# Optimization experiments

Hardware: AMD Instinct MI355X
Metric: run time of the kernel (lower is better)

## Reference

```python
import jax, jax.numpy as jnp
import numpy as np

B, L, D = 4, 4096, 128
BLOCK, SPARSITY = 64, 0.9
NEG = -1e9


def _make_block_mask(key):
    nb = L // BLOCK
    bm = jax.random.uniform(key, (nb, nb)) > SPARSITY
    bm = bm | jnp.eye(nb, dtype=bool)  # keep diagonal blocks so no row is fully masked
    bm = jnp.tril(bm)
    return jnp.repeat(jnp.repeat(bm, BLOCK, axis=0), BLOCK, axis=1)  # [L, L]


def _xavier(key, shape):
    limit = float(np.sqrt(6.0 / (shape[0] + shape[1])))
    return jax.random.uniform(key, shape, jnp.float32, -limit, limit)


def setup_inputs() -> dict:
    key = jax.random.key(0)
    ks = jax.random.split(key, 10)
    t = lambda k: jax.random.normal(k, (B, L, D), jnp.float32)
    return {
        'q_real': t(ks[0]), 'q_imag': t(ks[1]),
        'k_real': t(ks[2]), 'k_imag': t(ks[3]),
        'v_real': t(ks[4]), 'v_imag': t(ks[5]),
        'W_qkv': _xavier(ks[6], (6 * D, 6 * D)),
        'b_qkv': jnp.zeros((6 * D,), jnp.float32),
        'W_out': _xavier(ks[7], (2 * D, 2 * D)),
        'b_out': jnp.zeros((2 * D,), jnp.float32),
        'block_mask': _make_block_mask(ks[8]),
    }


def reference(q_real, q_imag, k_real, k_imag, v_real, v_imag,
              W_qkv, b_qkv, W_out, b_out, block_mask):
    d = q_real.shape[-1]
    scale = d ** -0.5
    # fused qkv projection over the 6 concatenated channels
    x = jnp.concatenate([q_real, q_imag, k_real, k_imag, v_real, v_imag], axis=-1)  # [B,L,6D]
    qkv = (x @ W_qkv.T + b_qkv).reshape(x.shape[0], x.shape[1], 6, d)
    q_r, q_i, k_r, k_i, v_r, v_i = (qkv[:, :, j] for j in range(6))

    def attn(q, k, v):
        s = jnp.einsum('bqd,bkd->bqk', q, k) * scale          # [B,L,L]
        s = jnp.where(block_mask[None], s, NEG)               # block-sparse mask
        a = jax.nn.softmax(s, axis=-1)                        # dropout = identity (eval)
        return jnp.einsum('bqk,bkd->bqd', a, v)

    out = jnp.concatenate([attn(q_r, k_r, v_r), attn(q_i, k_i, v_i)], axis=-1)  # [B,L,2D]
    out = out @ W_out.T + b_out
    return out[..., :d], out[..., d:]
```

## Files before the change

### kernel.cpp

```cpp
#include <hip/hip_runtime.h>
#include <hip/hip_bf16.h>

typedef unsigned short u16;
typedef __attribute__((ext_vector_type(8))) short bf16x8;
typedef __attribute__((ext_vector_type(4))) float f32x4;

#define SEQ_L 4096
#define M_TOT 16384

__device__ __forceinline__ float bf2f(u16 x) {
    unsigned u = ((unsigned)x) << 16;
    return __builtin_bit_cast(float, u);
}
__device__ __forceinline__ u16 f2bf(float f) {
    unsigned u = __builtin_bit_cast(unsigned, f);
    u += 0x7FFFu + ((u >> 16) & 1u);
    return (u16)(u >> 16);
}
__device__ __forceinline__ void gload16(const u16* g, u16* l) {
    __builtin_amdgcn_global_load_lds(
        (const __attribute__((address_space(1))) unsigned int*)g,
        (__attribute__((address_space(3))) unsigned int*)l, 16, 0, 0);
}

__global__ __launch_bounds__(256) void pack_x(
    const float* __restrict__ in0, const float* __restrict__ in1, const float* __restrict__ in2,
    const float* __restrict__ in3, const float* __restrict__ in4, const float* __restrict__ in5,
    u16* __restrict__ x) {
    const float* ins[6] = {in0, in1, in2, in3, in4, in5};
    int which = blockIdx.y;
    const float* src = ins[which];
    int g = blockIdx.x * 256 + threadIdx.x;
    int m = g >> 4, c8 = g & 15;
    const float* sp = src + (size_t)m * 128 + c8 * 8;
    float4 a = *(const float4*)sp;
    float4 b = *(const float4*)(sp + 4);
    u16 t[8] = {f2bf(a.x), f2bf(a.y), f2bf(a.z), f2bf(a.w),
                f2bf(b.x), f2bf(b.y), f2bf(b.z), f2bf(b.w)};
    *(uint4*)(x + (size_t)m * 768 + which * 128 + c8 * 8) = *(uint4*)t;
}

__global__ __launch_bounds__(256) void prep(
    const float* __restrict__ Wqkv, const float* __restrict__ Wout, const void* __restrict__ mask,
    u16* __restrict__ Wqkv_bf, u16* __restrict__ Wout_bf, unsigned char* __restrict__ cmask) {
    int id = blockIdx.x * 256 + threadIdx.x;
    if (id < 73728 + 8192) {
        const float* src = (id < 73728) ? Wqkv : Wout;
        u16* dst = (id < 73728) ? Wqkv_bf : Wout_bf;
        int i = (id < 73728) ? id : (id - 73728);
        const float* sp = src + (size_t)i * 8;
        float4 a = *(const float4*)sp;
        float4 b = *(const float4*)(sp + 4);
        u16 t[8] = {f2bf(a.x), f2bf(a.y), f2bf(a.z), f2bf(a.w),
                    f2bf(b.x), f2bf(b.y), f2bf(b.z), f2bf(b.w)};
        *(uint4*)(dst + (size_t)i * 8) = *(uint4*)t;
    } else if (id < 73728 + 8192 + 4096) {
        int i = id - 73728 - 8192;
        int bi = i >> 6, bj = i & 63;
        size_t e = (size_t)(bi * 64) * SEQ_L + (size_t)bj * 64;
        const unsigned char* p8 = (const unsigned char*)mask;
        unsigned w0 = *(const unsigned*)mask;
        bool v;
        if (w0 == 0x01010101u || w0 == 0xFFFFFFFFu)      v = p8[e] != 0;
        else if (w0 == 0x3F803F80u || w0 == 0x3C003C00u) v = ((const u16*)mask)[e] != 0;
        else                                             v = ((const unsigned*)mask)[e] != 0;
        cmask[i] = v ? 1 : 0;
    }
}

__global__ __launch_bounds__(256) void qkv_gemm(
    const u16* __restrict__ X, const u16* __restrict__ W, const float* __restrict__ bias,
    u16* __restrict__ qk, u16* __restrict__ vt) {
    __shared__ __align__(16) u16 As[128 * 64];
    __shared__ __align__(16) u16 Bs[128 * 64];
    int m0 = blockIdx.x * 128, n0 = blockIdx.y * 128;
    int tid = threadIdx.x, lane = tid & 63, w = tid >> 6;
    int ln = lane & 15, quad = lane >> 4;
    int rw = (w >> 1) * 64, cw = (w & 1) * 64;
    int lr8 = lane >> 3, lc = lane & 7;
    int swz_st = lc ^ (lr8 & 7);
    f32x4 acc[4][4] = {};
    for (int kk = 0; kk < 768; kk += 64) {
        __syncthreads();
        #pragma unroll
        for (int j = 0; j < 4; j++) {
            int r0 = w * 32 + j * 8;
            int r = r0 + lr8;
            gload16(X + (size_t)(m0 + r) * 768 + kk + swz_st * 8, As + r0 * 64 + lane * 8);
            gload16(W + (size_t)(n0 + r) * 768 + kk + swz_st * 8, Bs + r0 * 64 + lane * 8);
        }
        __syncthreads();
        #pragma unroll
        for (int s = 0; s < 2; s++) {
            bf16x8 af[4], bfr[4];
            #pragma unroll
            for (int i = 0; i < 4; i++) {
                int R = rw + i * 16 + ln;
                af[i] = *(const bf16x8*)(As + R * 64 + ((4 * s + quad) ^ (ln & 7)) * 8);
            }
            #pragma unroll
            for (int t = 0; t < 4; t++) {
                int R = cw + t * 16 + ln;
                bfr[t] = *(const bf16x8*)(Bs + R * 64 + ((4 * s + quad) ^ (ln & 7)) * 8);
            }
            #pragma unroll
            for (int i = 0; i < 4; i++)
                #pragma unroll
                for (int t = 0; t < 4; t++)
                    acc[i][t] = __builtin_amdgcn_mfma_f32_16x16x32_bf16(af[i], bfr[t], acc[i][t], 0, 0, 0);
        }
    }
    #pragma unroll
    for (int i = 0; i < 4; i++) {
        int row0 = m0 + rw + i * 16 + 4 * quad;
        #pragma unroll
        for (int t = 0; t < 4; t++) {
            int col = n0 + cw + t * 16 + ln;
            float bv = bias[col];
            if (col < 512) {
                #pragma unroll
                for (int r = 0; r < 4; r++)
                    qk[(size_t)(row0 + r) * 512 + col] = f2bf(acc[i][t][r] + bv);
            } else {
                int d = col - 512;
                int b = row0 >> 12, seq = row0 & 4095;
                u16 pk[4] = {f2bf(acc[i][t][0] + bv), f2bf(acc[i][t][1] + bv),
                             f2bf(acc[i][t][2] + bv), f2bf(acc[i][t][3] + bv)};
                *(ushort4*)(vt + ((size_t)(b * 2 + (d >> 7)) * 128 + (d & 127)) * SEQ_L + seq)
                    = *(ushort4*)pk;
            }
        }
    }
}

__global__ __launch_bounds__(256) void attn_kernel(
    const u16* __restrict__ qk, const u16* __restrict__ vt,
    const unsigned char* __restrict__ cmask, u16* __restrict__ attn_out) {
    __shared__ __align__(16) u16 Ks[2][64 * 128];
    __shared__ __align__(16) u16 Vt[2][128 * 64];
    __shared__ __align__(16) u16 Ps[4][16 * 72];

    int idx = blockIdx.x;
    int qi = 63 - (idx >> 3);
    int sub = idx & 7, c = sub & 1, b = sub >> 1;
    int tid = threadIdx.x, lane = tid & 63, w = tid >> 6;
    int ln = lane & 15, quad = lane >> 4;
    const float scale = 0.08838834764831845f;

    const u16* kb_base = qk + (size_t)b * SEQ_L * 512 + 256 + c * 128;
    const u16* vt_base = vt + (size_t)(b * 2 + c) * 128 * SEQ_L;

    int k_lr = lane >> 4, k_lc = lane & 15;
    int v_lr = lane >> 3, v_lc = lane & 7;

    bf16x8 qf[4];
    {
        size_t grow = (size_t)(b * SEQ_L + qi * 64 + w * 16 + ln);
        const u16* qp = qk + grow * 512 + c * 128;
        #pragma unroll
        for (int s = 0; s < 4; s++) qf[s] = *(const bf16x8*)(qp + 32 * s + 8 * quad);
    }
    float m_st[4], l_st[4];
    #pragma unroll
    for (int r = 0; r < 4; r++) { m_st[r] = -1e30f; l_st[r] = 0.f; }
    f32x4 accO[8] = {};

    const unsigned char* mrow = cmask + qi * 64;
    unsigned long long bm = 0;
    for (int k = 0; k <= qi; k++) bm |= (unsigned long long)(mrow[k] != 0) << k;

    int cur = __ffsll(bm) - 1; bm &= bm - 1;
    int buf = 0;
    {
        const u16* kp = kb_base + (size_t)cur * 64 * 512;
        const u16* vp = vt_base + cur * 64;
        #pragma unroll
        for (int j = 0; j < 4; j++) {
            int kr0 = w * 16 + j * 4, kr = kr0 + k_lr;
            gload16(kp + (size_t)kr * 512 + (k_lc ^ (kr & 7)) * 8, Ks[0] + kr0 * 128 + lane * 8);
            int vr0 = w * 32 + j * 8, vr = vr0 + v_lr;
            gload16(vp + (size_t)vr * SEQ_L + (v_lc ^ (vr & 7)) * 8, Vt[0] + vr0 * 64 + lane * 8);
        }
    }
    while (cur >= 0) {
        int nxt = bm ? (__ffsll(bm) - 1) : -1;
        if (bm) bm &= bm - 1;
        __syncthreads();
        if (nxt >= 0) {
            const u16* kp = kb_base + (size_t)nxt * 64 * 512;
            const u16* vp = vt_base + nxt * 64;
            #pragma unroll
            for (int j = 0; j < 4; j++) {
                int kr0 = w * 16 + j * 4, kr = kr0 + k_lr;
                gload16(kp + (size_t)kr * 512 + (k_lc ^ (kr & 7)) * 8, Ks[buf ^ 1] + kr0 * 128 + lane * 8);
                int vr0 = w * 32 + j * 8, vr = vr0 + v_lr;
                gload16(vp + (size_t)vr * SEQ_L + (v_lc ^ (vr & 7)) * 8, Vt[buf ^ 1] + vr0 * 64 + lane * 8);
            }
        }

        f32x4 accS[4] = {};
        #pragma unroll
        for (int s = 0; s < 4; s++) {
            #pragma unroll
            for (int t = 0; t < 4; t++) {
                int R = t * 16 + ln;
                bf16x8 bfr = *(const bf16x8*)(Ks[buf] + R * 128 + ((4 * s + quad) ^ (ln & 7)) * 8);
                accS[t] = __builtin_amdgcn_mfma_f32_16x16x32_bf16(qf[s], bfr, accS[t], 0, 0, 0);
            }
        }

        float P[4][4];
        #pragma unroll
        for (int r = 0; r < 4; r++) {
            float sv[4];
            float mx = -1e30f;
            #pragma unroll
            for (int t = 0; t < 4; t++) { sv[t] = accS[t][r] * scale; mx = fmaxf(mx, sv[t]); }
            #pragma unroll
            for (int off = 1; off < 16; off <<= 1) mx = fmaxf(mx, __shfl_xor(mx, off, 64));
            float nm = fmaxf(m_st[r], mx);
            float alpha = __expf(m_st[r] - nm);
            m_st[r] = nm;
            float rs = 0.f;
            #pragma unroll
            for (int t = 0; t < 4; t++) { float p = __expf(sv[t] - nm); P[t][r] = p; rs += p; }
            #pragma unroll
            for (int off = 1; off < 16; off <<= 1) rs += __shfl_xor(rs, off, 64);
            l_st[r] = l_st[r] * alpha + rs;
            #pragma unroll
            for (int nt = 0; nt < 8; nt++) accO[nt][r] *= alpha;
        }
        #pragma unroll
        for (int t = 0; t < 4; t++)
            #pragma unroll
            for (int r = 0; r < 4; r++)
                Ps[w][(4 * quad + r) * 72 + ln + 16 * t] = f2bf(P[t][r]);

        #pragma unroll
        for (int s2 = 0; s2 < 2; s2++) {
            bf16x8 pf = *(const bf16x8*)(&Ps[w][ln * 72 + 32 * s2 + 8 * quad]);
            #pragma unroll
            for (int nt = 0; nt < 8; nt++) {
                int R = nt * 16 + ln;
                bf16x8 vf = *(const bf16x8*)(Vt[buf] + R * 64 + ((4 * s2 + quad) ^ (ln & 7)) * 8);
                accO[nt] = __builtin_amdgcn_mfma_f32_16x16x32_bf16(pf, vf, accO[nt], 0, 0, 0);
            }
        }
        cur = nxt; buf ^= 1;
    }

    #pragma unroll
    for (int nt = 0; nt < 8; nt++) {
        int col = c * 128 + nt * 16 + ln;
        #pragma unroll
        for (int r = 0; r < 4; r++) {
            int row = b * SEQ_L + qi * 64 + w * 16 + 4 * quad + r;
            float inv = 1.0f / fmaxf(l_st[r], 1e-20f);
            attn_out[(size_t)row * 256 + col] = f2bf(accO[nt][r] * inv);
        }
    }
}

__global__ __launch_bounds__(256) void out_gemm(
    const u16* __restrict__ A, const u16* __restrict__ W, const float* __restrict__ bias,
    float* __restrict__ out) {
    __shared__ __align__(16) u16 As[64 * 64];
    __shared__ __align__(16) u16 Bs[64 * 64];
    int m0 = blockIdx.x * 64, n0 = blockIdx.y * 64;
    int tid = threadIdx.x, lane = tid & 63, w = tid >> 6;
    int ln = lane & 15, quad = lane >> 4;
    int lr8 = lane >> 3, lc = lane & 7;
    int swz_st = lc ^ (lr8 & 7);
    f32x4 acc[4] = {};
    for (int kk = 0; kk < 256; kk += 64) {
        __syncthreads();
        #pragma unroll
        for (int j = 0; j < 2; j++) {
            int r0 = w * 16 + j * 8;
            int r = r0 + lr8;
            gload16(A + (size_t)(m0 + r) * 256 + kk + swz_st * 8, As + r0 * 64 + lane * 8);
            gload16(W + (size_t)(n0 + r) * 256 + kk + swz_st * 8, Bs + r0 * 64 + lane * 8);
        }
        __syncthreads();
        #pragma unroll
        for (int s = 0; s < 2; s++) {
            int R = w * 16 + ln;
            bf16x8 af = *(const bf16x8*)(As + R * 64 + ((4 * s + quad) ^ (ln & 7)) * 8);
            #pragma unroll
            for (int t = 0; t < 4; t++) {
                int Rb = t * 16 + ln;
                bf16x8 bfr = *(const bf16x8*)(Bs + Rb * 64 + ((4 * s + quad) ^ (ln & 7)) * 8);
                acc[t] = __builtin_amdgcn_mfma_f32_16x16x32_bf16(af, bfr, acc[t], 0, 0, 0);
            }
        }
    }
    const size_t half = (size_t)M_TOT * 128;
    #pragma unroll
    for (int t = 0; t < 4; t++) {
        int col = n0 + t * 16 + ln;
        float bv = bias[col];
        float* base = (col < 128) ? (out + col) : (out + half + (col - 128));
        #pragma unroll
        for (int r = 0; r < 4; r++) {
            int row = m0 + w * 16 + 4 * quad + r;
            base[(size_t)row * 128] = acc[t][r] + bv;
        }
    }
}

extern "C" void kernel_launch(void* const* d_in, const int* in_sizes, int n_in,
                              void* d_out, int out_size, void* d_ws, size_t ws_size,
                              hipStream_t stream) {
    char* ws = (char*)d_ws;
    u16* x_bf    = (u16*)ws;
    u16* qk_buf  = x_bf + (size_t)M_TOT * 768;
    u16* vt_buf  = qk_buf + (size_t)M_TOT * 512;
    u16* attn_bf = vt_buf + (size_t)1024 * SEQ_L;
    u16* Wqkv_bf = attn_bf + (size_t)M_TOT * 256;
    u16* Wout_bf = Wqkv_bf + 589824;
    unsigned char* cmask = (unsigned char*)(Wout_bf + 65536);

    hipLaunchKernelGGL(pack_x, dim3(1024, 6), dim3(256), 0, stream,
                       (const float*)d_in[0], (const float*)d_in[1], (const float*)d_in[2],
                       (const float*)d_in[3], (const float*)d_in[4], (const float*)d_in[5], x_bf);
    hipLaunchKernelGGL(prep, dim3(336), dim3(256), 0, stream,
                       (const float*)d_in[6], (const float*)d_in[8], d_in[10],
                       Wqkv_bf, Wout_bf, cmask);
    hipLaunchKernelGGL(qkv_gemm, dim3(128, 6), dim3(256), 0, stream,
                       x_bf, Wqkv_bf, (const float*)d_in[7], qk_buf, vt_buf);
    hipLaunchKernelGGL(attn_kernel, dim3(512), dim3(256), 0, stream,
                       qk_buf, vt_buf, cmask, attn_bf);
    hipLaunchKernelGGL(out_gemm, dim3(256, 4), dim3(256), 0, stream,
                       attn_bf, Wout_bf, (const float*)d_in[9], (float*)d_out);
}
```

Baseline: 224.0 us.

## Fuse output projection into attention kernel and merge prep kernels

The attention kernel now processes both real and imaginary channels per block, keeping the normalized output in shared memory, then performs the output projection with W_out directly and writes fp32 results. The separate out_gemm kernel and the bf16 attention intermediate buffer are removed, and pack_x and prep are combined into one launch. This saves a launch and an HBM round trip of the attention output. In exchange, the grid halves to 256 blocks with serialized per-channel work, and the larger shared memory footprint can lower occupancy, so load balance across CUs may get worse.

```diff
diff --git a/kernel.cpp b/kernel.cpp
--- a/kernel.cpp
+++ b/kernel.cpp
@@ -23,39 +23,36 @@
         (__attribute__((address_space(3))) unsigned int*)l, 16, 0, 0);
 }
 
-__global__ __launch_bounds__(256) void pack_x(
+__global__ __launch_bounds__(256) void prep_all(
     const float* __restrict__ in0, const float* __restrict__ in1, const float* __restrict__ in2,
     const float* __restrict__ in3, const float* __restrict__ in4, const float* __restrict__ in5,
-    u16* __restrict__ x) {
-    const float* ins[6] = {in0, in1, in2, in3, in4, in5};
-    int which = blockIdx.y;
-    const float* src = ins[which];
-    int g = blockIdx.x * 256 + threadIdx.x;
-    int m = g >> 4, c8 = g & 15;
-    const float* sp = src + (size_t)m * 128 + c8 * 8;
-    float4 a = *(const float4*)sp;
-    float4 b = *(const float4*)(sp + 4);
-    u16 t[8] = {f2bf(a.x), f2bf(a.y), f2bf(a.z), f2bf(a.w),
-                f2bf(b.x), f2bf(b.y), f2bf(b.z), f2bf(b.w)};
-    *(uint4*)(x + (size_t)m * 768 + which * 128 + c8 * 8) = *(uint4*)t;
-}
-
-__global__ __launch_bounds__(256) void prep(
     const float* __restrict__ Wqkv, const float* __restrict__ Wout, const void* __restrict__ mask,
-    u16* __restrict__ Wqkv_bf, u16* __restrict__ Wout_bf, unsigned char* __restrict__ cmask) {
+    u16* __restrict__ x, u16* __restrict__ Wqkv_bf, u16* __restrict__ Wout_bf,
+    unsigned char* __restrict__ cmask) {
     int id = blockIdx.x * 256 + threadIdx.x;
-    if (id < 73728 + 8192) {
-        const float* src = (id < 73728) ? Wqkv : Wout;
-        u16* dst = (id < 73728) ? Wqkv_bf : Wout_bf;
-        int i = (id < 73728) ? id : (id - 73728);
+    if (id < 1572864) {
+        const float* ins[6] = {in0, in1, in2, in3, in4, in5};
+        int which = id >> 18, j = id & 262143;
+        int m = j >> 4, c8 = j & 15;
+        const float* sp = ins[which] + (size_t)m * 128 + c8 * 8;
+        float4 a = *(const float4*)sp;
+        float4 b = *(const float4*)(sp + 4);
+        u16 t[8] = {f2bf(a.x), f2bf(a.y), f2bf(a.z), f2bf(a.w),
+                    f2bf(b.x), f2bf(b.y), f2bf(b.z), f2bf(b.w)};
+        *(uint4*)(x + (size_t)m * 768 + which * 128 + c8 * 8) = *(uint4*)t;
+    } else if (id < 1572864 + 73728 + 8192) {
+        int i = id - 1572864;
+        const float* src = (i < 73728) ? Wqkv : Wout;
+        u16* dst = (i < 73728) ? Wqkv_bf : Wout_bf;
+        if (i >= 73728) i -= 73728;
         const float* sp = src + (size_t)i * 8;
         float4 a = *(const float4*)sp;
         float4 b = *(const float4*)(sp + 4);
         u16 t[8] = {f2bf(a.x), f2bf(a.y), f2bf(a.z), f2bf(a.w),
                     f2bf(b.x), f2bf(b.y), f2bf(b.z), f2bf(b.w)};
         *(uint4*)(dst + (size_t)i * 8) = *(uint4*)t;
-    } else if (id < 73728 + 8192 + 4096) {
-        int i = id - 73728 - 8192;
+    } else if (id < 1572864 + 73728 + 8192 + 4096) {
+        int i = id - 1572864 - 73728 - 8192;
         int bi = i >> 6, bj = i & 63;
         size_t e = (size_t)(bi * 64) * SEQ_L + (size_t)bj * 64;
         const unsigned char* p8 = (const unsigned char*)mask;
@@ -133,177 +130,177 @@
     }
 }
 
-__global__ __launch_bounds__(256) void attn_kernel(
-    const u16* __restrict__ qk, const u16* __restrict__ vt,
-    const unsigned char* __restrict__ cmask, u16* __restrict__ attn_out) {
+__global__ __launch_bounds__(256) void attn_out(
+    const u16* __restrict__ qk, const u16* __restrict__ vt, const u16* __restrict__ Wout,
+    const unsigned char* __restrict__ cmask, const float* __restrict__ bout,
+    float* __restrict__ out) {
     __shared__ __align__(16) u16 Ks[2][64 * 128];
     __shared__ __align__(16) u16 Vt[2][128 * 64];
     __shared__ __align__(16) u16 Ps[4][16 * 72];
+    __shared__ __align__(16) u16 Ao[64 * 264];
 
     int idx = blockIdx.x;
-    int qi = 63 - (idx >> 3);
-    int sub = idx & 7, c = sub & 1, b = sub >> 1;
+    int qi = 63 - (idx >> 2);
+    int b = idx & 3;
     int tid = threadIdx.x, lane = tid & 63, w = tid >> 6;
     int ln = lane & 15, quad = lane >> 4;
     const float scale = 0.08838834764831845f;
 
-    const u16* kb_base = qk + (size_t)b * SEQ_L * 512 + 256 + c * 128;
-    const u16* vt_base = vt + (size_t)(b * 2 + c) * 128 * SEQ_L;
-
     int k_lr = lane >> 4, k_lc = lane & 15;
     int v_lr = lane >> 3, v_lc = lane & 7;
 
-    bf16x8 qf[4];
-    {
-        size_t grow = (size_t)(b * SEQ_L + qi * 64 + w * 16 + ln);
-        const u16* qp = qk + grow * 512 + c * 128;
-        #pragma unroll
-        for (int s = 0; s < 4; s++) qf[s] = *(const bf16x8*)(qp + 32 * s + 8 * quad);
-    }
-    float m_st[4], l_st[4];
-    #pragma unroll
-    for (int r = 0; r < 4; r++) { m_st[r] = -1e30f; l_st[r] = 0.f; }
-    f32x4 accO[8] = {};
-
     const unsigned char* mrow = cmask + qi * 64;
-    unsigned long long bm = 0;
-    for (int k = 0; k <= qi; k++) bm |= (unsigned long long)(mrow[k] != 0) << k;
-
-    int cur = __ffsll(bm) - 1; bm &= bm - 1;
-    int buf = 0;
-    {
-        const u16* kp = kb_base + (size_t)cur * 64 * 512;
-        const u16* vp = vt_base + cur * 64;
-        #pragma unroll
-        for (int j = 0; j < 4; j++) {
-            int kr0 = w * 16 + j * 4, kr = kr0 + k_lr;
-            gload16(kp + (size_t)kr * 512 + (k_lc ^ (kr & 7)) * 8, Ks[0] + kr0 * 128 + lane * 8);
-            int vr0 = w * 32 + j * 8, vr = vr0 + v_lr;
-            gload16(vp + (size_t)vr * SEQ_L + (v_lc ^ (vr & 7)) * 8, Vt[0] + vr0 * 64 + lane * 8);
-        }
-    }
-    while (cur >= 0) {
-        int nxt = bm ? (__ffsll(bm) - 1) : -1;
-        if (bm) bm &= bm - 1;
-        __syncthreads();
-        if (nxt >= 0) {
-            const u16* kp = kb_base + (size_t)nxt * 64 * 512;
-            const u16* vp = vt_base + nxt * 64;
+    unsigned long long bm0 = 0;
+    for (int k = 0; k <= qi; k++) bm0 |= (unsigned long long)(mrow[k] != 0) << k;
+
+    for (int c = 0; c < 2; c++) {
+        const u16* kb_base = qk + (size_t)b * SEQ_L * 512 + 256 + c * 128;
+        const u16* vt_base = vt + (size_t)(b * 2 + c) * 128 * SEQ_L;
+
+        bf16x8 qf[4];
+        {
+            size_t grow = (size_t)(b * SEQ_L + qi * 64 + w * 16 + ln);
+            const u16* qp = qk + grow * 512 + c * 128;
+            #pragma unroll
+            for (int s = 0; s < 4; s++) qf[s] = *(const bf16x8*)(qp + 32 * s + 8 * quad);
+        }
+        float m_st[4], l_st[4];
+        #pragma unroll
+        for (int r = 0; r < 4; r++) { m_st[r] = -1e30f; l_st[r] = 0.f; }
+        f32x4 accO[8] = {};
+
+        unsigned long long bm = bm0;
+        int cur = __ffsll(bm) - 1; bm &= bm - 1;
+        int buf = 0;
+        __syncthreads();
+        {
+            const u16* kp = kb_base + (size_t)cur * 64 * 512;
+            const u16* vp = vt_base + cur * 64;
             #pragma unroll
             for (int j = 0; j < 4; j++) {
                 int kr0 = w * 16 + j * 4, kr = kr0 + k_lr;
-                gload16(kp + (size_t)kr * 512 + (k_lc ^ (kr & 7)) * 8, Ks[buf ^ 1] + kr0 * 128 + lane * 8);
+                gload16(kp + (size_t)kr * 512 + (k_lc ^ (kr & 7)) * 8, Ks[0] + kr0 * 128 + lane * 8);
                 int vr0 = w * 32 + j * 8, vr = vr0 + v_lr;
-                gload16(vp + (size_t)vr * SEQ_L + (v_lc ^ (vr & 7)) * 8, Vt[buf ^ 1] + vr0 * 64 + lane * 8);
-            }
-        }
-
-        f32x4 accS[4] = {};
-        #pragma unroll
-        for (int s = 0; s < 4; s++) {
+                gload16(vp + (size_t)vr * SEQ_L + (v_lc ^ (vr & 7)) * 8, Vt[0] + vr0 * 64 + lane * 8);
+            }
+        }
+        while (cur >= 0) {
+            int nxt = bm ? (__ffsll(bm) - 1) : -1;
+            if (bm) bm &= bm - 1;
+            __syncthreads();
+            if (nxt >= 0) {
+                const u16* kp = kb_base + (size_t)nxt * 64 * 512;
+                const u16* vp = vt_base + nxt * 64;
+                #pragma unroll
+                for (int j = 0; j < 4; j++) {
+                    int kr0 = w * 16 + j * 4, kr = kr0 + k_lr;
+                    gload16(kp + (size_t)kr * 512 + (k_lc ^ (kr & 7)) * 8, Ks[buf ^ 1] + kr0 * 128 + lane * 8);
+                    int vr0 = w * 32 + j * 8, vr = vr0 + v_lr;
+                    gload16(vp + (size_t)vr * SEQ_L + (v_lc ^ (vr & 7)) * 8, Vt[buf ^ 1] + vr0 * 64 + lane * 8);
+                }
+            }
+
+            f32x4 accS[4] = {};
+            #pragma unroll
+            for (int s = 0; s < 4; s++) {
+                #pragma unroll
+                for (int t = 0; t < 4; t++) {
+                    int R = t * 16 + ln;
+                    bf16x8 bfr = *(const bf16x8*)(Ks[buf] + R * 128 + ((4 * s + quad) ^ (ln & 7)) * 8);
+                    accS[t] = __builtin_amdgcn_mfma_f32_16x16x32_bf16(qf[s], bfr, accS[t], 0, 0, 0);
+                }
+            }
+            float P[4][4];
+            #pragma unroll
+            for (int r = 0; r < 4; r++) {
+                float sv[4];
+                float mx = -1e30f;
+                #pragma unroll
+                for (int t = 0; t < 4; t++) { sv[t] = accS[t][r] * scale; mx = fmaxf(mx, sv[t]); }
+                #pragma unroll
+                for (int off = 1; off < 16; off <<= 1) mx = fmaxf(mx, __shfl_xor(mx, off, 64));
+                float nm = fmaxf(m_st[r], mx);
+                float alpha = __expf(m_st[r] - nm);
+                m_st[r] = nm;
+                float rs = 0.f;
+                #pragma unroll
+                for (int t = 0; t < 4; t++) { float p = __expf(sv[t] - nm); P[t][r] = p; rs += p; }
+                #pragma unroll
+                for (int off = 1; off < 16; off <<= 1) rs += __shfl_xor(rs, off, 64);
+                l_st[r] = l_st[r] * alpha + rs;
+                #pragma unroll
+                for (int nt = 0; nt < 8; nt++) accO[nt][r] *= alpha;
+            }
+            #pragma unroll
+            for (int t = 0; t < 4; t++)
+                #pragma unroll
+                for (int r = 0; r < 4; r++)
+                    Ps[w][(4 * quad + r) * 72 + ln + 16 * t] = f2bf(P[t][r]);
+            #pragma unroll
+            for (int s2 = 0; s2 < 2; s2++) {
+                bf16x8 pf = *(const bf16x8*)(&Ps[w][ln * 72 + 32 * s2 + 8 * quad]);
+                #pragma unroll
+                for (int nt = 0; nt < 8; nt++) {
+                    int R = nt * 16 + ln;
+                    bf16x8 vf = *(const bf16x8*)(Vt[buf] + R * 64 + ((4 * s2 + quad) ^ (ln & 7)) * 8);
+                    accO[nt] = __builtin_amdgcn_mfma_f32_16x16x32_bf16(pf, vf, accO[nt], 0, 0, 0);
+                }
+            }
+            cur = nxt; buf ^= 1;
+        }
+        float inv[4];
+        #pragma unroll
+        for (int r = 0; r < 4; r++) inv[r] = 1.0f / fmaxf(l_st[r], 1e-20f);
+        #pragma unroll
+        for (int nt = 0; nt < 8; nt++)
+            #pragma unroll
+            for (int r = 0; r < 4; r++)
+                Ao[(w * 16 + 4 * quad + r) * 264 + c * 128 + nt * 16 + ln]
+                    = f2bf(accO[nt][r] * inv[r]);
+    }
+
+    u16* Bs = Ks[0];
+    f32x4 oacc[4][4] = {};
+    for (int kk = 0; kk < 4; kk++) {
+        __syncthreads();
+        #pragma unroll
+        for (int j = 0; j < 8; j++) {
+            int o0 = w * 64 + j * 8;
+            int o = o0 + (lane >> 3);
+            gload16(Wout + (size_t)o * 256 + kk * 64 + (((lane & 7) ^ (o & 7)) * 8),
+                    Bs + o0 * 64 + lane * 8);
+        }
+        __syncthreads();
+        #pragma unroll
+        for (int s = 0; s < 2; s++) {
+            bf16x8 af[4], bfr[4];
+            #pragma unroll
+            for (int i = 0; i < 4; i++)
+                af[i] = *(const bf16x8*)(Ao + (i * 16 + ln) * 264 + kk * 64 + 32 * s + 8 * quad);
             #pragma unroll
             for (int t = 0; t < 4; t++) {
-                int R = t * 16 + ln;
-                bf16x8 bfr = *(const bf16x8*)(Ks[buf] + R * 128 + ((4 * s + quad) ^ (ln & 7)) * 8);
-                accS[t] = __builtin_amdgcn_mfma_f32_16x16x32_bf16(qf[s], bfr, accS[t], 0, 0, 0);
-            }
-        }
-
-        float P[4][4];
-        #pragma unroll
-        for (int r = 0; r < 4; r++) {
-            float sv[4];
-            float mx = -1e30f;
-            #pragma unroll
-            for (int t = 0; t < 4; t++) { sv[t] = accS[t][r] * scale; mx = fmaxf(mx, sv[t]); }
-            #pragma unroll
-            for (int off = 1; off < 16; off <<= 1) mx = fmaxf(mx, __shfl_xor(mx, off, 64));
-            float nm = fmaxf(m_st[r], mx);
-            float alpha = __expf(m_st[r] - nm);
-            m_st[r] = nm;
-            float rs = 0.f;
-            #pragma unroll
-            for (int t = 0; t < 4; t++) { float p = __expf(sv[t] - nm); P[t][r] = p; rs += p; }
-            #pragma unroll
-            for (int off = 1; off < 16; off <<= 1) rs += __shfl_xor(rs, off, 64);
-            l_st[r] = l_st[r] * alpha + rs;
-            #pragma unroll
-            for (int nt = 0; nt < 8; nt++) accO[nt][r] *= alpha;
-        }
-        #pragma unroll
-        for (int t = 0; t < 4; t++)
-            #pragma unroll
-            for (int r = 0; r < 4; r++)
-                Ps[w][(4 * quad + r) * 72 + ln + 16 * t] = f2bf(P[t][r]);
-
-        #pragma unroll
-        for (int s2 = 0; s2 < 2; s2++) {
-            bf16x8 pf = *(const bf16x8*)(&Ps[w][ln * 72 + 32 * s2 + 8 * quad]);
-            #pragma unroll
-            for (int nt = 0; nt < 8; nt++) {
-                int R = nt * 16 + ln;
-                bf16x8 vf = *(const bf16x8*)(Vt[buf] + R * 64 + ((4 * s2 + quad) ^ (ln & 7)) * 8);
-                accO[nt] = __builtin_amdgcn_mfma_f32_16x16x32_bf16(pf, vf, accO[nt], 0, 0, 0);
-            }
-        }
-        cur = nxt; buf ^= 1;
-    }
-
-    #pragma unroll
-    for (int nt = 0; nt < 8; nt++) {
-        int col = c * 128 + nt * 16 + ln;
-        #pragma unroll
-        for (int r = 0; r < 4; r++) {
-            int row = b * SEQ_L + qi * 64 + w * 16 + 4 * quad + r;
-            float inv = 1.0f / fmaxf(l_st[r], 1e-20f);
-            attn_out[(size_t)row * 256 + col] = f2bf(accO[nt][r] * inv);
-        }
-    }
-}
-
-__global__ __launch_bounds__(256) void out_gemm(
-    const u16* __restrict__ A, const u16* __restrict__ W, const float* __restrict__ bias,
-    float* __restrict__ out) {
-    __shared__ __align__(16) u16 As[64 * 64];
-    __shared__ __align__(16) u16 Bs[64 * 64];
-    int m0 = blockIdx.x * 64, n0 = blockIdx.y * 64;
-    int tid = threadIdx.x, lane = tid & 63, w = tid >> 6;
-    int ln = lane & 15, quad = lane >> 4;
-    int lr8 = lane >> 3, lc = lane & 7;
-    int swz_st = lc ^ (lr8 & 7);
-    f32x4 acc[4] = {};
-    for (int kk = 0; kk < 256; kk += 64) {
-        __syncthreads();
-        #pragma unroll
-        for (int j = 0; j < 2; j++) {
-            int r0 = w * 16 + j * 8;
-            int r = r0 + lr8;
-            gload16(A + (size_t)(m0 + r) * 256 + kk + swz_st * 8, As + r0 * 64 + lane * 8);
-            gload16(W + (size_t)(n0 + r) * 256 + kk + swz_st * 8, Bs + r0 * 64 + lane * 8);
-        }
-        __syncthreads();
-        #pragma unroll
-        for (int s = 0; s < 2; s++) {
-            int R = w * 16 + ln;
-            bf16x8 af = *(const bf16x8*)(As + R * 64 + ((4 * s + quad) ^ (ln & 7)) * 8);
-            #pragma unroll
-            for (int t = 0; t < 4; t++) {
-                int Rb = t * 16 + ln;
-                bf16x8 bfr = *(const bf16x8*)(Bs + Rb * 64 + ((4 * s + quad) ^ (ln & 7)) * 8);
-                acc[t] = __builtin_amdgcn_mfma_f32_16x16x32_bf16(af, bfr, acc[t], 0, 0, 0);
-            }
+                int o = w * 64 + t * 16 + ln;
+                bfr[t] = *(const bf16x8*)(Bs + o * 64 + ((4 * s + quad) ^ (ln & 7)) * 8);
+            }
+            #pragma unroll
+            for (int i = 0; i < 4; i++)
+                #pragma unroll
+                for (int t = 0; t < 4; t++)
+                    oacc[i][t] = __builtin_amdgcn_mfma_f32_16x16x32_bf16(af[i], bfr[t], oacc[i][t], 0, 0, 0);
         }
     }
     const size_t half = (size_t)M_TOT * 128;
     #pragma unroll
     for (int t = 0; t < 4; t++) {
-        int col = n0 + t * 16 + ln;
-        float bv = bias[col];
-        float* base = (col < 128) ? (out + col) : (out + half + (col - 128));
-        #pragma unroll
-        for (int r = 0; r < 4; r++) {
-            int row = m0 + w * 16 + 4 * quad + r;
-            base[(size_t)row * 128] = acc[t][r] + bv;
+        int o = w * 64 + t * 16 + ln;
+        float bv = bout[o];
+        float* base = (o < 128) ? (out + o) : (out + half + (o - 128));
+        #pragma unroll
+        for (int i = 0; i < 4; i++) {
+            int row = b * SEQ_L + qi * 64 + i * 16 + 4 * quad;
+            #pragma unroll
+            for (int r = 0; r < 4; r++)
+                base[(size_t)(row + r) * 128] = oacc[i][t][r] + bv;
         }
     }
 }
@@ -315,21 +312,17 @@
     u16* x_bf    = (u16*)ws;
     u16* qk_buf  = x_bf + (size_t)M_TOT * 768;
     u16* vt_buf  = qk_buf + (size_t)M_TOT * 512;
-    u16* attn_bf = vt_buf + (size_t)1024 * SEQ_L;
-    u16* Wqkv_bf = attn_bf + (size_t)M_TOT * 256;
+    u16* Wqkv_bf = vt_buf + (size_t)1024 * SEQ_L;
     u16* Wout_bf = Wqkv_bf + 589824;
     unsigned char* cmask = (unsigned char*)(Wout_bf + 65536);
 
-    hipLaunchKernelGGL(pack_x, dim3(1024, 6), dim3(256), 0, stream,
+    hipLaunchKernelGGL(prep_all, dim3(6480), dim3(256), 0, stream,
                        (const float*)d_in[0], (const float*)d_in[1], (const float*)d_in[2],
-                       (const float*)d_in[3], (const float*)d_in[4], (const float*)d_in[5], x_bf);
-    hipLaunchKernelGGL(prep, dim3(336), dim3(256), 0, stream,
+                       (const float*)d_in[3], (const float*)d_in[4], (const float*)d_in[5],
                        (const float*)d_in[6], (const float*)d_in[8], d_in[10],
-                       Wqkv_bf, Wout_bf, cmask);
+                       x_bf, Wqkv_bf, Wout_bf, cmask);
     hipLaunchKernelGGL(qkv_gemm, dim3(128, 6), dim3(256), 0, stream,
                        x_bf, Wqkv_bf, (const float*)d_in[7], qk_buf, vt_buf);
-    hipLaunchKernelGGL(attn_kernel, dim3(512), dim3(256), 0, stream,
-                       qk_buf, vt_buf, cmask, attn_bf);
-    hipLaunchKernelGGL(out_gemm, dim3(256, 4), dim3(256), 0, stream,
-                       attn_bf, Wout_bf, (const float*)d_in[9], (float*)d_out);
-}
+    hipLaunchKernelGGL(attn_out, dim3(256), dim3(256), 0, stream,
+                       qk_buf, vt_buf, Wout_bf, cmask, (const float*)d_in[9], (float*)d_out);
+}
```

Measured after the change: 242.8 us. 8.4% more time.
